# Kernel tuning notes

Hardware: AMD Instinct MI355X
Metric: run time of the kernel (lower is better)

## Reference

```python
import jax, jax.numpy as jnp
import numpy as np


def _h(s):
    # Step function: 0 where s > 0, else 1 (zero gradient everywhere).
    return jnp.where(s > 0, 0.0, 1.0).astype(s.dtype)


def setup_inputs() -> dict:
    key = jax.random.key(0)
    k1, k2, k3 = jax.random.split(key, 3)
    B, T = 4096, 2048
    x = jax.random.normal(k1, (B, T, 1), dtype=jnp.float32)
    out_prev = jax.random.normal(k2, (B, 1, 1), dtype=jnp.float32)
    lstm_outs = jax.random.normal(k3, (B, T, 4), dtype=jnp.float32)
    return {"x": x, "out_prev": out_prev, "lstm_outs": lstm_outs}


def reference(x, out_prev, lstm_outs):
    # x: [B, T, 1], out_prev: [B, 1, 1] (only first step used), lstm_outs: [B, T, 4]
    xT = jnp.swapaxes(x, 0, 1)          # [T, B, 1]
    wT = jnp.swapaxes(lstm_outs, 0, 1)  # [T, B, 4]

    def step(prev, inputs):
        # prev: [B, 1]
        xt, wt = inputs                  # [B, 1], [B, 4]
        m_lo = wt[:, 0:1]
        m_up = wt[:, 1:2]
        c_lo = wt[:, 2:3]
        c_up = wt[:, 3:4]
        # h() arguments use detached weights in the original (grad is zero through
        # the step function anyway); stop_gradient kept for faithfulness.
        m_lo_d = jax.lax.stop_gradient(m_lo)
        m_up_d = jax.lax.stop_gradient(m_up)
        c_lo_d = jax.lax.stop_gradient(c_lo)
        c_up_d = jax.lax.stop_gradient(c_up)
        f1 = _h((m_lo_d * xt + m_lo_d * c_lo_d - prev) / m_lo_d)
        f2 = _h((prev - m_up_d * xt - m_up_d * c_up_d) / m_up_d)
        out = (m_lo * xt * f1 + m_lo * c_lo * f1
               + m_up * xt * f2 + m_up * c_up * f2
               + prev * (1.0 - f1) * (1.0 - f2))
        return out, out

    init = out_prev[:, 0, :]             # [B, 1]
    _, outs = jax.lax.scan(step, init, (xT, wT))  # outs: [T, B, 1]
    custom_output = jnp.swapaxes(outs, 0, 1)      # [B, T, 1]
    # Original also returns (lstm_outs, 0, 0, 0) passthrough; main output is below.
    return custom_output
```

## Files before the change

kernel.cpp:

```cpp
#include <hip/hip_runtime.h>


#define C 64
#define NCH 32
#define NTB 3
#define NOB 4
#define TS 65
#define XS 68

#define CFENCE() asm volatile("" ::: "memory")

__global__ __launch_bounds__(192) void pc_scan(
    const float* __restrict__ x, const float* __restrict__ p0,
    const float4* __restrict__ lstm4, float* __restrict__ out,
    int B, int T) {
#pragma clang fp contract(off)
  __shared__ float4 tileA[NTB][16 * TS];
  __shared__ float4 tileB[NTB][16 * TS];
  __shared__ float xt[16 * XS];
  __shared__ float ostg[NOB][16 * XS];
  __shared__ int stagedw[2][NCH];
  __shared__ int scanned;

  const int tid = threadIdx.x;
  const int b0 = blockIdx.x * 16;
  const float4* x4 = reinterpret_cast<const float4*>(x);
  float4* out4 = reinterpret_cast<float4*>(out);

  for (int i = tid; i < 2 * NCH; i += 192) ((int*)stagedw)[i] = 0;
  if (tid == 0) scanned = 0;
  __syncthreads();

  if (tid >= 64) {
    const int q = tid - 64;
    const int pj = (q >> 3) & 15;
    const int pk = q & 7;
    const int w = (tid >> 6) - 1;
    const bool lead = (q & 63) == 0;

    float4 L00, L01, L02, L03, L04, L05, L06, L07;
    float4 L10, L11, L12, L13, L14, L15, L16, L17;
    float4 X00, X01, X10, X11;

#define ISSUE(S, CH)                                                    \
  {                                                                     \
    size_t rb = (size_t)(b0 + pj) * T + (size_t)(CH) * C;               \
    const float4* lp = lstm4 + rb + pk;                                 \
    L##S##0 = lp[0];  L##S##1 = lp[8];  L##S##2 = lp[16];               \
    L##S##3 = lp[24]; L##S##4 = lp[32]; L##S##5 = lp[40];               \
    L##S##6 = lp[48]; L##S##7 = lp[56];                                 \
    X##S##0 = x4[(rb >> 2) + 2 * pk];                                   \
    X##S##1 = x4[(rb >> 2) + 2 * pk + 1];                               \
  }

#define STAGE_ELT(LV, SS, BUF)                                          \
  {                                                                     \
    float4 wv = LV;                       \
    float xv = xt[pj * XS + (SS)];                                      \
    float a1 = wv.x * xv, a2 = wv.x * wv.z;                             \
    float L1v = a1 + a2;                                                \
    unsigned s1m = __float_as_uint(wv.x) & 0x80000000u;                 \
    float L1f = __uint_as_float(__float_as_uint(L1v) ^ s1m);            \
    float a3 = wv.y * xv, a4 = wv.y * wv.w;                             \
    unsigned f2m = (__float_as_uint(wv.y) & 0x80000000u) ^ 0x80000000u; \
    float a3f = __uint_as_float(__float_as_uint(a3) ^ f2m);             \
    float a4f = __uint_as_float(__float_as_uint(a4) ^ f2m);             \
    float V01 = a3 + a4;                                                \
    float V11 = (L1v + a3) + a4;                                        \
    tileA[BUF][pj * TS + (SS)] =                                        \
        make_float4(__uint_as_float(s1m), L1f, __uint_as_float(f2m), a3f); \
    tileB[BUF][pj * TS + (SS)] = make_float4(a4f, V11, V01, L1v);       \
  }

#define STAGE(S, BUF)                                                   \
  {                                                                     \
    *(float4*)&xt[pj * XS + 8 * pk] = X##S##0;                          \
    *(float4*)&xt[pj * XS + 8 * pk + 4] = X##S##1;                      \
    STAGE_ELT(L##S##0, pk,      BUF)                                    \
    STAGE_ELT(L##S##1, pk + 8,  BUF)                                    \
    STAGE_ELT(L##S##2, pk + 16, BUF)                                    \
    STAGE_ELT(L##S##3, pk + 24, BUF)                                    \
    STAGE_ELT(L##S##4, pk + 32, BUF)                                    \
    STAGE_ELT(L##S##5, pk + 40, BUF)                                    \
    STAGE_ELT(L##S##6, pk + 48, BUF)                                    \
    STAGE_ELT(L##S##7, pk + 56, BUF)                                    \
  }

#define FLUSH(CP, OB)                                                   \
  {                                                                     \
    float4 v0 = *(const float4*)&ostg[OB][pj * XS + 8 * pk];            \
    float4 v1 = *(const float4*)&ostg[OB][pj * XS + 8 * pk + 4];        \
    size_t ob = ((size_t)(b0 + pj) * T + (size_t)(CP) * C) >> 2;        \
    out4[ob + 2 * pk] = v0;                                             \
    out4[ob + 2 * pk + 1] = v1;                                         \
  }

#define PWAIT(TGT)                                                      \
  while (*(volatile int*)&scanned < (TGT)) __builtin_amdgcn_s_sleep(1); \
  CFENCE();

    ISSUE(0, 0)
    ISSUE(1, 1)

    for (int k = 0; k < NCH; k += 2) {
      PWAIT(k - 2)
      STAGE(0, k % NTB)
      CFENCE();
      if (lead) *(volatile int*)&stagedw[w][k] = 1;
      if (k + 2 < NCH) ISSUE(0, k + 2)
      if (k >= 3) FLUSH(k - 3, (k - 3) % NOB)
      PWAIT(k - 1)
      STAGE(1, (k + 1) % NTB)
      CFENCE();
      if (lead) *(volatile int*)&stagedw[w][k + 1] = 1;
      if (k + 3 < NCH) ISSUE(1, k + 3)
      if (k >= 2) FLUSH(k - 2, (k - 2) % NOB)
    }
    for (int j = NCH - 3; j < NCH; ++j) {
      PWAIT(j + 1)
      FLUSH(j, j % NOB)
    }
  } else {
    float p = (tid < 16) ? p0[b0 + tid] : 0.0f;

#define RSTEP(I, OVC)                                                   \
  {                                                                     \
    float4 A = rA##I;                                                   \
    float4 Bv = rB##I;                                                  \
    if (g < 7) {                                                        \
      rA##I = ta[8 * g + 8 + I];                                        \
      rB##I = tb[8 * g + 8 + I];                                        \
    }                                                                   \
    unsigned pu = __float_as_uint(p);                                   \
    float pf = __uint_as_float(pu ^ __float_as_uint(A.x));              \
    bool c1 = pf >= A.y;                                                \
    float pp = __uint_as_float(pu ^ __float_as_uint(A.z));              \
    float qv = pp - A.w;                                                \
    bool c2 = qv >= Bv.x;                                               \
    float i1 = c1 ? Bv.y : Bv.z;                                        \
    float i2 = c1 ? Bv.w : p;                                           \
    p = c2 ? i1 : i2;                                                   \
    OVC = p;                                                            \
  }

    for (int c = 0; c < NCH; ++c) {
      for (;;) {
        int a = *(volatile int*)&stagedw[0][c];
        int b = *(volatile int*)&stagedw[1][c];
        if (a + b == 2) break;
        __builtin_amdgcn_s_sleep(1);
      }
      CFENCE();
      if (tid < 16) {
        const float4* ta = &tileA[c % NTB][tid * TS];
        const float4* tb = &tileB[c % NTB][tid * TS];
        float* orow = &ostg[c % NOB][tid * XS];
        float4 rA0 = ta[0], rA1 = ta[1], rA2 = ta[2], rA3 = ta[3];
        float4 rA4 = ta[4], rA5 = ta[5], rA6 = ta[6], rA7 = ta[7];
        float4 rB0 = tb[0], rB1 = tb[1], rB2 = tb[2], rB3 = tb[3];
        float4 rB4 = tb[4], rB5 = tb[5], rB6 = tb[6], rB7 = tb[7];
#pragma unroll
        for (int g = 0; g < 8; ++g) {
          float4 ov0, ov1;
          RSTEP(0, ov0.x) RSTEP(1, ov0.y) RSTEP(2, ov0.z) RSTEP(3, ov0.w)
          RSTEP(4, ov1.x) RSTEP(5, ov1.y) RSTEP(6, ov1.z) RSTEP(7, ov1.w)
          *(float4*)&orow[8 * g] = ov0;
          *(float4*)&orow[8 * g + 4] = ov1;
        }
      }
      CFENCE();
      if (tid == 0) *(volatile int*)&scanned = c + 1;
    }
  }
}

extern "C" void kernel_launch(void* const* d_in, const int* in_sizes, int n_in,
                              void* d_out, int out_size, void* d_ws, size_t ws_size,
                              hipStream_t stream) {
  const float* x = (const float*)d_in[0];
  const float* op = (const float*)d_in[1];
  const float4* lstm = (const float4*)d_in[2];
  int B = in_sizes[1];
  int T = in_sizes[0] / B;
  hipLaunchKernelGGL(pc_scan, dim3(B / 16), dim3(192), 0, stream,
                     x, op, lstm, (float*)d_out, B, T);
}
```

Baseline: 231.3 us.

## Interleave tile layout and write scan outputs directly to global memory

Merges the A/B staging tiles into one interleaved slot per timestep and has producers read x as scalars straight from global memory, which removes the x staging buffer. The 16 scan threads now write outputs directly to global memory, so the output staging buffers and the producer-side flush are gone. The scan loop is software-pipelined across groups of 8 steps with even/odd register sets and per-chunk spin waits without sleep. Four tile buffers give producers a deeper lead. The trade-offs are strided scalar x loads, narrow global stores from only 16 lanes, and busy-wait polling.

```diff
diff --git a/kernel.cpp b/kernel.cpp
--- a/kernel.cpp
+++ b/kernel.cpp
@@ -3,10 +3,9 @@
 
 #define C 64
 #define NCH 32
-#define NTB 3
-#define NOB 4
-#define TS 65
-#define XS 68
+#define NTB 4
+#define RS 129
+#define SLOT (16 * RS)
 
 #define CFENCE() asm volatile("" ::: "memory")
 
@@ -15,48 +14,48 @@
     const float4* __restrict__ lstm4, float* __restrict__ out,
     int B, int T) {
 #pragma clang fp contract(off)
-  __shared__ float4 tileA[NTB][16 * TS];
-  __shared__ float4 tileB[NTB][16 * TS];
-  __shared__ float xt[16 * XS];
-  __shared__ float ostg[NOB][16 * XS];
-  __shared__ int stagedw[2][NCH];
+  __shared__ float4 tile[NTB][SLOT];
+  __shared__ int stg[NCH][2];
   __shared__ int scanned;
 
   const int tid = threadIdx.x;
   const int b0 = blockIdx.x * 16;
-  const float4* x4 = reinterpret_cast<const float4*>(x);
   float4* out4 = reinterpret_cast<float4*>(out);
-
-  for (int i = tid; i < 2 * NCH; i += 192) ((int*)stagedw)[i] = 0;
+  (void)B;
+
+  for (int i = tid; i < 2 * NCH; i += 192) ((int*)stg)[i] = 0;
   if (tid == 0) scanned = 0;
   __syncthreads();
 
   if (tid >= 64) {
     const int q = tid - 64;
-    const int pj = (q >> 3) & 15;
+    const int pj = q >> 3;
     const int pk = q & 7;
-    const int w = (tid >> 6) - 1;
+    const int w = q >> 6;
     const bool lead = (q & 63) == 0;
 
     float4 L00, L01, L02, L03, L04, L05, L06, L07;
     float4 L10, L11, L12, L13, L14, L15, L16, L17;
-    float4 X00, X01, X10, X11;
+    float x00, x01, x02, x03, x04, x05, x06, x07;
+    float x10, x11, x12, x13, x14, x15, x16, x17;
 
 #define ISSUE(S, CH)                                                    \
   {                                                                     \
     size_t rb = (size_t)(b0 + pj) * T + (size_t)(CH) * C;               \
     const float4* lp = lstm4 + rb + pk;                                 \
+    const float* xp = x + rb + pk;                                      \
     L##S##0 = lp[0];  L##S##1 = lp[8];  L##S##2 = lp[16];               \
     L##S##3 = lp[24]; L##S##4 = lp[32]; L##S##5 = lp[40];               \
     L##S##6 = lp[48]; L##S##7 = lp[56];                                 \
-    X##S##0 = x4[(rb >> 2) + 2 * pk];                                   \
-    X##S##1 = x4[(rb >> 2) + 2 * pk + 1];                               \
-  }
-
-#define STAGE_ELT(LV, SS, BUF)                                          \
+    x##S##0 = xp[0];  x##S##1 = xp[8];  x##S##2 = xp[16];               \
+    x##S##3 = xp[24]; x##S##4 = xp[32]; x##S##5 = xp[40];               \
+    x##S##6 = xp[48]; x##S##7 = xp[56];                                 \
+  }
+
+#define STAGE_ELT(LV, XV, TW, OFF)                                      \
   {                                                                     \
     float4 wv = LV;                       \
-    float xv = xt[pj * XS + (SS)];                                      \
+    float xv = XV;                                                      \
     float a1 = wv.x * xv, a2 = wv.x * wv.z;                             \
     float L1v = a1 + a2;                                                \
     unsigned s1m = __float_as_uint(wv.x) & 0x80000000u;                 \
@@ -67,32 +66,22 @@
     float a4f = __uint_as_float(__float_as_uint(a4) ^ f2m);             \
     float V01 = a3 + a4;                                                \
     float V11 = (L1v + a3) + a4;                                        \
-    tileA[BUF][pj * TS + (SS)] =                                        \
-        make_float4(__uint_as_float(s1m), L1f, __uint_as_float(f2m), a3f); \
-    tileB[BUF][pj * TS + (SS)] = make_float4(a4f, V11, V01, L1v);       \
+    (TW)[OFF] = make_float4(__uint_as_float(s1m), L1f,                  \
+                            __uint_as_float(f2m), a3f);                 \
+    (TW)[(OFF) + 1] = make_float4(a4f, V11, V01, L1v);                  \
   }
 
 #define STAGE(S, BUF)                                                   \
   {                                                                     \
-    *(float4*)&xt[pj * XS + 8 * pk] = X##S##0;                          \
-    *(float4*)&xt[pj * XS + 8 * pk + 4] = X##S##1;                      \
-    STAGE_ELT(L##S##0, pk,      BUF)                                    \
-    STAGE_ELT(L##S##1, pk + 8,  BUF)                                    \
-    STAGE_ELT(L##S##2, pk + 16, BUF)                                    \
-    STAGE_ELT(L##S##3, pk + 24, BUF)                                    \
-    STAGE_ELT(L##S##4, pk + 32, BUF)                                    \
-    STAGE_ELT(L##S##5, pk + 40, BUF)                                    \
-    STAGE_ELT(L##S##6, pk + 48, BUF)                                    \
-    STAGE_ELT(L##S##7, pk + 56, BUF)                                    \
-  }
-
-#define FLUSH(CP, OB)                                                   \
-  {                                                                     \
-    float4 v0 = *(const float4*)&ostg[OB][pj * XS + 8 * pk];            \
-    float4 v1 = *(const float4*)&ostg[OB][pj * XS + 8 * pk + 4];        \
-    size_t ob = ((size_t)(b0 + pj) * T + (size_t)(CP) * C) >> 2;        \
-    out4[ob + 2 * pk] = v0;                                             \
-    out4[ob + 2 * pk + 1] = v1;                                         \
+    float4* tw = &tile[BUF][pj * RS + 2 * pk];                          \
+    STAGE_ELT(L##S##0, x##S##0, tw, 0)                                  \
+    STAGE_ELT(L##S##1, x##S##1, tw, 16)                                 \
+    STAGE_ELT(L##S##2, x##S##2, tw, 32)                                 \
+    STAGE_ELT(L##S##3, x##S##3, tw, 48)                                 \
+    STAGE_ELT(L##S##4, x##S##4, tw, 64)                                 \
+    STAGE_ELT(L##S##5, x##S##5, tw, 80)                                 \
+    STAGE_ELT(L##S##6, x##S##6, tw, 96)                                 \
+    STAGE_ELT(L##S##7, x##S##7, tw, 112)                                \
   }
 
 #define PWAIT(TGT)                                                      \
@@ -103,34 +92,48 @@
     ISSUE(1, 1)
 
     for (int k = 0; k < NCH; k += 2) {
+      PWAIT(k - 3)
+      STAGE(0, k & 3)
+      CFENCE();
+      if (lead) *(volatile int*)&stg[k][w] = 1;
+      if (k + 2 < NCH) ISSUE(0, k + 2)
       PWAIT(k - 2)
-      STAGE(0, k % NTB)
+      STAGE(1, (k + 1) & 3)
       CFENCE();
-      if (lead) *(volatile int*)&stagedw[w][k] = 1;
-      if (k + 2 < NCH) ISSUE(0, k + 2)
-      if (k >= 3) FLUSH(k - 3, (k - 3) % NOB)
-      PWAIT(k - 1)
-      STAGE(1, (k + 1) % NTB)
-      CFENCE();
-      if (lead) *(volatile int*)&stagedw[w][k + 1] = 1;
+      if (lead) *(volatile int*)&stg[k + 1][w] = 1;
       if (k + 3 < NCH) ISSUE(1, k + 3)
-      if (k >= 2) FLUSH(k - 2, (k - 2) % NOB)
     }
-    for (int j = NCH - 3; j < NCH; ++j) {
-      PWAIT(j + 1)
-      FLUSH(j, j % NOB)
-    }
-  } else {
-    float p = (tid < 16) ? p0[b0 + tid] : 0.0f;
-
-#define RSTEP(I, OVC)                                                   \
-  {                                                                     \
-    float4 A = rA##I;                                                   \
-    float4 Bv = rB##I;                                                  \
-    if (g < 7) {                                                        \
-      rA##I = ta[8 * g + 8 + I];                                        \
-      rB##I = tb[8 * g + 8 + I];                                        \
-    }                                                                   \
+  } else if (tid < 16) {
+    const int row = tid;
+    float p = p0[b0 + row];
+    float4* op = out4 + (((size_t)(b0 + row) * T) >> 2);
+    const float4* base0 = &tile[0][row * RS];
+    const float4* slotb = base0;
+    const float4* gp;
+
+    float4 rA0E, rA1E, rA2E, rA3E, rA4E, rA5E, rA6E, rA7E;
+    float4 rB0E, rB1E, rB2E, rB3E, rB4E, rB5E, rB6E, rB7E;
+    float4 rA0O, rA1O, rA2O, rA3O, rA4O, rA5O, rA6O, rA7O;
+    float4 rB0O, rB1O, rB2O, rB3O, rB4O, rB5O, rB6O, rB7O;
+
+#define CWAIT(CC)                                                       \
+  for (;;) {                                                            \
+    int fa = *(volatile int*)&stg[CC][0];                               \
+    int fb = *(volatile int*)&stg[CC][1];                               \
+    if (fa + fb == 2) break;                                            \
+  }                                                                     \
+  CFENCE();
+
+#define LOADG(S, P)                                                     \
+  rA0##S = (P)[0];  rB0##S = (P)[1];  rA1##S = (P)[2];  rB1##S = (P)[3];\
+  rA2##S = (P)[4];  rB2##S = (P)[5];  rA3##S = (P)[6];  rB3##S = (P)[7];\
+  rA4##S = (P)[8];  rB4##S = (P)[9];  rA5##S = (P)[10]; rB5##S = (P)[11];\
+  rA6##S = (P)[12]; rB6##S = (P)[13]; rA7##S = (P)[14]; rB7##S = (P)[15];
+
+#define RSTEP(S, I, OV)                                                 \
+  {                                                                     \
+    float4 A = rA##I##S;                                                \
+    float4 Bv = rB##I##S;                                               \
     unsigned pu = __float_as_uint(p);                                   \
     float pf = __uint_as_float(pu ^ __float_as_uint(A.x));              \
     bool c1 = pf >= A.y;                                                \
@@ -140,37 +143,47 @@
     float i1 = c1 ? Bv.y : Bv.z;                                        \
     float i2 = c1 ? Bv.w : p;                                           \
     p = c2 ? i1 : i2;                                                   \
-    OVC = p;                                                            \
-  }
-
-    for (int c = 0; c < NCH; ++c) {
-      for (;;) {
-        int a = *(volatile int*)&stagedw[0][c];
-        int b = *(volatile int*)&stagedw[1][c];
-        if (a + b == 2) break;
-        __builtin_amdgcn_s_sleep(1);
-      }
-      CFENCE();
-      if (tid < 16) {
-        const float4* ta = &tileA[c % NTB][tid * TS];
-        const float4* tb = &tileB[c % NTB][tid * TS];
-        float* orow = &ostg[c % NOB][tid * XS];
-        float4 rA0 = ta[0], rA1 = ta[1], rA2 = ta[2], rA3 = ta[3];
-        float4 rA4 = ta[4], rA5 = ta[5], rA6 = ta[6], rA7 = ta[7];
-        float4 rB0 = tb[0], rB1 = tb[1], rB2 = tb[2], rB3 = tb[3];
-        float4 rB4 = tb[4], rB5 = tb[5], rB6 = tb[6], rB7 = tb[7];
-#pragma unroll
-        for (int g = 0; g < 8; ++g) {
-          float4 ov0, ov1;
-          RSTEP(0, ov0.x) RSTEP(1, ov0.y) RSTEP(2, ov0.z) RSTEP(3, ov0.w)
-          RSTEP(4, ov1.x) RSTEP(5, ov1.y) RSTEP(6, ov1.z) RSTEP(7, ov1.w)
-          *(float4*)&orow[8 * g] = ov0;
-          *(float4*)&orow[8 * g + 4] = ov1;
-        }
-      }
-      CFENCE();
-      if (tid == 0) *(volatile int*)&scanned = c + 1;
+    OV = p;                                                             \
+  }
+
+#define BODY(CUR, NXT, CG, LAST)                                        \
+  {                                                                     \
+    const int cg_ = (CG);                                               \
+    if (!(LAST)) {                                                      \
+      int ncg = cg_ + 1;                                                \
+      const float4* np;                                                 \
+      if ((ncg & 7) == 0) {                                             \
+        int nc = ncg >> 3;                                              \
+        CWAIT(nc)                                                       \
+        slotb = ((nc & 3) == 0) ? base0 : (slotb + SLOT);               \
+        np = slotb;                                                     \
+      } else {                                                          \
+        np = gp + 16;                                                   \
+      }                                                                 \
+      LOADG(NXT, np)                                                    \
+      gp = np;                                                          \
+    }                                                                   \
+    float4 ov0, ov1;                                                    \
+    RSTEP(CUR, 0, ov0.x) RSTEP(CUR, 1, ov0.y)                           \
+    RSTEP(CUR, 2, ov0.z) RSTEP(CUR, 3, ov0.w)                           \
+    RSTEP(CUR, 4, ov1.x) RSTEP(CUR, 5, ov1.y)                           \
+    RSTEP(CUR, 6, ov1.z) RSTEP(CUR, 7, ov1.w)                           \
+    op[0] = ov0;                                                        \
+    op[1] = ov1;                                                        \
+    op += 2;                                                            \
+    if (((cg_) & 7) == 7 && row == 0)                                   \
+      *(volatile int*)&scanned = (cg_ >> 3) + 1;                        \
+  }
+
+    CWAIT(0)
+    gp = base0;
+    LOADG(E, gp)
+    for (int it = 0; it < 127; ++it) {
+      BODY(E, O, 2 * it, 0)
+      BODY(O, E, 2 * it + 1, 0)
     }
+    BODY(E, O, 254, 0)
+    BODY(O, E, 255, 1)
   }
 }
 
```

New measurement: 248.1 us. 1.07x slower.
